# Optimization experiments

Hardware: AMD Instinct MI355X
Metric: run time of the kernel (lower is better)

## Reference

```python
import jax, jax.numpy as jnp
import numpy as np
from jax import lax

B, L, ENC_IN, MARK = 8, 512, 7, 4
D_MODEL, EXPAND, D_STATE, D_CONV = 512, 2, 16, 4
D_INNER = D_MODEL * EXPAND
DT_RANK = int(np.ceil(D_MODEL / 16))  # 32
PRED_LEN, C_OUT = 96, 7


def _positional_embedding(seq_len, d_model):
    pos = jnp.arange(seq_len, dtype=jnp.float32)[:, None]
    div = jnp.exp(jnp.arange(0, d_model, 2, dtype=jnp.float32) * (-np.log(10000.0) / d_model))
    pe = jnp.zeros((seq_len, d_model), dtype=jnp.float32)
    pe = pe.at[:, 0::2].set(jnp.sin(pos * div))
    pe = pe.at[:, 1::2].set(jnp.cos(pos * div))
    return pe  # [L, d_model]


def setup_inputs() -> dict:
    key = jax.random.key(0)
    ks = jax.random.split(key, 20)
    s = 0.02
    inp = {
        "x_enc": jax.random.normal(ks[0], (B, L, ENC_IN), jnp.float32),
        "x_mark_enc": jax.random.normal(ks[1], (B, L, MARK), jnp.float32),
        "x_dec": jax.random.normal(ks[2], (B, 144, ENC_IN), jnp.float32),
        "x_mark_dec": jax.random.normal(ks[3], (B, 144, MARK), jnp.float32),
        # DataEmbedding params
        "token_conv_w": jax.random.normal(ks[4], (D_MODEL, ENC_IN, 3), jnp.float32) * s,
        "temporal_w": jax.random.normal(ks[5], (D_MODEL, MARK), jnp.float32) * s,
        # Mamba params
        "in_proj_w": jax.random.normal(ks[6], (2 * D_INNER, D_MODEL), jnp.float32) * s,
        "conv1d_w": jax.random.normal(ks[7], (D_INNER, 1, D_CONV), jnp.float32) * s,
        "conv1d_b": jnp.zeros((D_INNER,), jnp.float32),
        "x_proj_w": jax.random.normal(ks[8], (DT_RANK + 2 * D_STATE, D_INNER), jnp.float32) * s,
        "dt_proj_w": jax.random.normal(ks[9], (D_INNER, DT_RANK), jnp.float32) * s,
        "dt_proj_b": jax.random.normal(ks[10], (D_INNER,), jnp.float32) * s,
        "A_log": jnp.log(jnp.broadcast_to(jnp.arange(1, D_STATE + 1, dtype=jnp.float32), (D_INNER, D_STATE))),
        "D_param": jnp.ones((D_INNER,), jnp.float32),
        "out_proj_w": jax.random.normal(ks[11], (D_MODEL, D_INNER), jnp.float32) * s,
        # prediction head
        "head_w": jax.random.normal(ks[12], (PRED_LEN * C_OUT, D_MODEL), jnp.float32) * s,
        "head_b": jnp.zeros((PRED_LEN * C_OUT,), jnp.float32),
    }
    return inp


def reference(x_enc, x_mark_enc, x_dec, x_mark_dec, token_conv_w, temporal_w,
              in_proj_w, conv1d_w, conv1d_b, x_proj_w, dt_proj_w, dt_proj_b,
              A_log, D_param, out_proj_w, head_w, head_b):
    # --- instance normalization (mean/std detached as in torch) ---
    mean_enc = lax.stop_gradient(jnp.mean(x_enc, axis=1, keepdims=True))       # [B,1,C]
    xc = x_enc - mean_enc
    std_enc = lax.stop_gradient(jnp.sqrt(jnp.var(xc, axis=1, keepdims=True) + 1e-5))
    xn = xc / std_enc                                                          # [B,L,C]

    # --- DataEmbedding: circular conv token emb + timeF linear + sinusoidal PE ---
    xp = jnp.pad(xn, ((0, 0), (1, 1), (0, 0)), mode="wrap")                    # circular pad on L
    val = lax.conv_general_dilated(xp.transpose(0, 2, 1), token_conv_w, (1,), "VALID")  # [B,D,L]
    val = val.transpose(0, 2, 1)                                               # [B,L,D]
    temp = x_mark_enc @ temporal_w.T                                           # [B,L,D]
    x = val + temp + _positional_embedding(L, D_MODEL)[None]                   # [B,L,D]

    # --- Mamba block ---
    xz = x @ in_proj_w.T                                                       # [B,L,2*Di]
    x_part, z = jnp.split(xz, 2, axis=-1)
    # causal depthwise conv over time
    xt = jnp.pad(x_part.transpose(0, 2, 1), ((0, 0), (0, 0), (D_CONV - 1, 0)))
    xconv = lax.conv_general_dilated(xt, conv1d_w, (1,), "VALID",
                                     feature_group_count=D_INNER) + conv1d_b[None, :, None]
    u = jax.nn.silu(xconv.transpose(0, 2, 1))                                  # [B,L,Di]

    dbl = u @ x_proj_w.T                                                       # [B,L,dt_rank+2n]
    dt_low = dbl[..., :DT_RANK]
    Bm = dbl[..., DT_RANK:DT_RANK + D_STATE]                                   # [B,L,n]
    Cm = dbl[..., DT_RANK + D_STATE:]                                          # [B,L,n]
    dt = jax.nn.softplus(dt_low @ dt_proj_w.T + dt_proj_b)                     # [B,L,Di]

    A = -jnp.exp(A_log)                                                        # [Di,n]
    deltaA = jnp.exp(dt[..., None] * A)                                        # [B,L,Di,n]
    deltaBu = dt[..., None] * Bm[:, :, None, :] * u[..., None]                 # [B,L,Di,n]

    def step(h, inputs):
        dA_t, dBu_t, c_t = inputs                                              # [B,Di,n],[B,Di,n],[B,n]
        h = dA_t * h + dBu_t
        y_t = jnp.einsum("bdn,bn->bd", h, c_t)
        return h, y_t

    h0 = jnp.zeros((B, D_INNER, D_STATE), dtype=x.dtype)
    _, ys = lax.scan(step, h0, (deltaA.transpose(1, 0, 2, 3),
                                deltaBu.transpose(1, 0, 2, 3),
                                Cm.transpose(1, 0, 2)))
    y = ys.transpose(1, 0, 2) + u * D_param                                    # [B,L,Di]
    y = y * jax.nn.silu(z)
    x_out = y @ out_proj_w.T                                                   # [B,L,D]

    # --- prediction head on last hidden state ---
    last = x_out[:, -1, :]                                                     # [B,D]
    pred = (last @ head_w.T + head_b).reshape(-1, PRED_LEN, C_OUT)
    return pred * std_enc + mean_enc
```

## Files before the change

kernel.cpp:

```cpp
#include <hip/hip_runtime.h>
#include <hip/hip_bf16.h>
#include <math.h>

#define BB 8
#define LL 512
#define CIN 7
#define MARKN 4
#define DM 512
#define DI 1024
#define DSN 16
#define NOUTC 672
#define NTC 8

typedef unsigned short ushortT;
typedef __attribute__((ext_vector_type(8))) short short8v;
typedef __attribute__((ext_vector_type(4))) float f32x4;

__device__ __forceinline__ float bf2f(ushortT u){ return __uint_as_float(((unsigned)u)<<16); }
__device__ __forceinline__ ushortT f2bf(float f){ __hip_bfloat16 h = __float2bfloat16(f); return *(ushortT*)&h; }

__global__ __launch_bounds__(256) void k_prep(const float* __restrict__ w_in,
    const float* __restrict__ xpw, const float* __restrict__ xe,
    ushortT* __restrict__ wbf, ushortT* __restrict__ xpwbf,
    float* __restrict__ mean, float* __restrict__ stdv, float* __restrict__ xn){
  int blk = blockIdx.x, tid = threadIdx.x;
  if(blk < 1024){
    int i = (blk*256 + tid)*4;
    float4 v = *(const float4*)(w_in + i);
    ushort4 pk; pk.x=f2bf(v.x); pk.y=f2bf(v.y); pk.z=f2bf(v.z); pk.w=f2bf(v.w);
    *(ushort4*)(wbf + i) = pk;
  } else if(blk < 1088){
    int i = ((blk-1024)*256 + tid)*4;
    float4 v = *(const float4*)(xpw + i);
    ushort4 pk; pk.x=f2bf(v.x); pk.y=f2bf(v.y); pk.z=f2bf(v.z); pk.w=f2bf(v.w);
    *(ushort4*)(xpwbf + i) = pk;
  } else if(tid < 64){
    int bc = blk - 1088;
    int b = bc / CIN, c = bc % CIN;
    int t = tid;
    const float* base = xe + (b*LL)*CIN + c;
    float v[8]; float s = 0.f;
    #pragma unroll
    for(int i=0;i<8;i++){ v[i] = base[(t + i*64)*CIN]; s += v[i]; }
    #pragma unroll
    for(int o=32;o>=1;o>>=1) s += __shfl_down(s, o);
    float m = __shfl(s, 0) * (1.0f/LL);
    float vs = 0.f;
    #pragma unroll
    for(int i=0;i<8;i++){ float dv = v[i]-m; vs += dv*dv; }
    #pragma unroll
    for(int o=32;o>=1;o>>=1) vs += __shfl_down(vs, o);
    float var = __shfl(vs, 0) * (1.0f/LL);
    float sd = sqrtf(var + 1e-5f);
    float inv = 1.0f / sd;
    if(t == 0){ mean[bc] = m; stdv[bc] = sd; }
    float* xnb = xn + (b*LL)*CIN + c;
    #pragma unroll
    for(int i=0;i<8;i++) xnb[(t + i*64)*CIN] = (v[i]-m)*inv;
  }
}

__global__ __launch_bounds__(512) void k_embed(const float* __restrict__ xn,
    const float* __restrict__ xmark, const float* __restrict__ tw,
    const float* __restrict__ tpw, __hip_bfloat16* __restrict__ xo){
  __shared__ float sw[DM*21];
  __shared__ float sxr[10][CIN];
  __shared__ float smr[8][MARKN];
  int blk = blockIdx.x;
  int b = blk >> 6;
  int l0 = (blk & 63) << 3;
  int tid = threadIdx.x;
  for(int i=tid; i<DM*21; i+=512) sw[i] = tw[i];
  if(tid < 70){
    int r = tid / CIN, c = tid % CIN;
    int ls = (l0 - 1 + r + LL) % LL;
    sxr[r][c] = xn[(b*LL + ls)*CIN + c];
  } else if(tid >= 128 && tid < 160){
    int i2 = tid - 128; int r = i2 >> 2, m = i2 & 3;
    smr[r][m] = xmark[(b*LL + l0 + r)*MARKN + m];
  }
  __syncthreads();
  int d = tid;
  float wv[21];
  #pragma unroll
  for(int i=0;i<21;i++) wv[i] = sw[d*21 + i];
  float tv[4];
  #pragma unroll
  for(int m=0;m<4;m++) tv[m] = tpw[d*MARKN + m];
  float divv = expf((float)(2*(d>>1)) * (-0.0179889460390159843f));
  bool isodd = (d & 1) != 0;
  #pragma unroll
  for(int ll=0; ll<8; ll++){
    float acc = 0.f;
    #pragma unroll
    for(int c=0;c<CIN;c++){
      #pragma unroll
      for(int k=0;k<3;k++) acc += sxr[ll+k][c] * wv[c*3+k];
    }
    #pragma unroll
    for(int m=0;m<4;m++) acc += smr[ll][m] * tv[m];
    float ang = (float)(l0+ll) * divv;
    acc += isodd ? cosf(ang) : sinf(ang);
    xo[(size_t)(b*LL + l0 + ll)*DM + d] = __float2bfloat16(acc);
  }
}

__global__ __launch_bounds__(256) void k_inproj_mfma(const ushortT* __restrict__ A,
    const ushortT* __restrict__ Bw, ushortT* __restrict__ C){
  __shared__ ushortT Asl[2][128*64];
  __shared__ ushortT Bsl[2][128*64];
  int tid = threadIdx.x;
  int w = tid >> 6, l = tid & 63;
  int m0 = blockIdx.y * 128, n0 = blockIdx.x * 128;
  int wr = w >> 1, wc = w & 1;
  f32x4 acc[4][4] = {};
  int srow = l >> 3;
  int scolswz = ((l & 7) * 16) ^ (srow << 4);

#define IP_STAGE(bufi, kt) do{ \
    _Pragma("unroll") \
    for(int i=0;i<4;i++){ \
      int r0 = w*32 + i*8; \
      int r = r0 + srow; \
      const ushortT* gA = A + (size_t)(m0 + r)*512 + (kt)*64 + (scolswz>>1); \
      const ushortT* gB = Bw + (size_t)(n0 + r)*512 + (kt)*64 + (scolswz>>1); \
      __builtin_amdgcn_global_load_lds( \
        (const __attribute__((address_space(1))) unsigned int*)(const void*)gA, \
        (__attribute__((address_space(3))) unsigned int*)(void*)(Asl[bufi] + r0*64), 16, 0, 0); \
      __builtin_amdgcn_global_load_lds( \
        (const __attribute__((address_space(1))) unsigned int*)(const void*)gB, \
        (__attribute__((address_space(3))) unsigned int*)(void*)(Bsl[bufi] + r0*64), 16, 0, 0); \
    } }while(0)

  IP_STAGE(0, 0);
  __syncthreads();
  int cur = 0;
  for(int kt = 0; kt < 8; ++kt){
    if(kt < 7) IP_STAGE(cur^1, kt+1);
    #pragma unroll
    for(int kk=0;kk<2;kk++){
      short8v af[4], bfr[4];
      int cb = kk*64 + (l>>4)*16;
      #pragma unroll
      for(int mf=0;mf<4;mf++){
        int ar = wr*64 + mf*16 + (l&15);
        af[mf] = *(const short8v*)(Asl[cur] + ar*64 + ((cb ^ ((ar&7)<<4))>>1));
      }
      #pragma unroll
      for(int nf=0;nf<4;nf++){
        int br = wc*64 + nf*16 + (l&15);
        bfr[nf] = *(const short8v*)(Bsl[cur] + br*64 + ((cb ^ ((br&7)<<4))>>1));
      }
      #pragma unroll
      for(int mf=0;mf<4;mf++)
        #pragma unroll
        for(int nf=0;nf<4;nf++)
          acc[mf][nf] = __builtin_amdgcn_mfma_f32_16x16x32_bf16(af[mf], bfr[nf], acc[mf][nf], 0, 0, 0);
    }
    __syncthreads();
    cur ^= 1;
  }
#undef IP_STAGE
  #pragma unroll
  for(int mf=0;mf<4;mf++){
    int rbase = m0 + wr*64 + mf*16 + (l>>4)*4;
    #pragma unroll
    for(int nf=0;nf<4;nf++){
      int col = n0 + wc*64 + nf*16 + (l&15);
      #pragma unroll
      for(int r=0;r<4;r++)
        C[(size_t)(rbase+r)*1024 + col] = f2bf(acc[mf][nf][r]);
    }
  }
}

__global__ __launch_bounds__(1024) void k_dwconv(const ushortT* __restrict__ xpbf,
    const float* __restrict__ cw, const float* __restrict__ cb,
    ushortT* __restrict__ ubf){
  int blk = blockIdx.x;
  int b = blk >> 5, l0 = (blk & 31) * 16;
  int d = threadIdx.x;
  const float4 w4 = *(const float4*)(cw + d*4);
  float bias = cb[d];
  const ushortT* base = xpbf + (size_t)(b*LL + l0)*1024 + d;
  float x0=0.f, x1=0.f, x2=0.f;
  if(l0 > 0){
    x0 = bf2f(base[-3*1024]); x1 = bf2f(base[-2*1024]); x2 = bf2f(base[-1*1024]);
  }
  #pragma unroll
  for(int ll=0; ll<16; ++ll){
    float x3 = bf2f(base[(size_t)ll*1024]);
    float acc = bias + x0*w4.x + x1*w4.y + x2*w4.z + x3*w4.w;
    float s = acc / (1.f + __expf(-acc));
    ubf[(size_t)(b*LL + l0 + ll)*1024 + d] = f2bf(s);
    x0 = x1; x1 = x2; x2 = x3;
  }
}

__global__ __launch_bounds__(256) void k_xproj_mfma(const ushortT* __restrict__ A,
    const ushortT* __restrict__ Bw, float* __restrict__ C){
  __shared__ ushortT Asl[2][64*64];
  __shared__ ushortT Bsl[2][64*64];
  int tid = threadIdx.x;
  int w = tid >> 6, l = tid & 63;
  int m0 = blockIdx.x * 64;
  f32x4 acc[4] = {};
  int srow = l >> 3;
  int scol = ((l & 7) * 16) ^ (srow << 4);

#define XP_STAGE(bufi, kt) do{ \
    _Pragma("unroll") \
    for(int i=0;i<2;i++){ \
      int r0 = w*16 + i*8; \
      int r = r0 + srow; \
      const ushortT* gA = A + (size_t)(m0 + r)*1024 + (kt)*64 + (scol>>1); \
      const ushortT* gB = Bw + (size_t)r*1024 + (kt)*64 + (scol>>1); \
      __builtin_amdgcn_global_load_lds( \
        (const __attribute__((address_space(1))) unsigned int*)(const void*)gA, \
        (__attribute__((address_space(3))) unsigned int*)(void*)(Asl[bufi] + r0*64), 16, 0, 0); \
      __builtin_amdgcn_global_load_lds( \
        (const __attribute__((address_space(1))) unsigned int*)(const void*)gB, \
        (__attribute__((address_space(3))) unsigned int*)(void*)(Bsl[bufi] + r0*64), 16, 0, 0); \
    } }while(0)

  XP_STAGE(0, 0);
  __syncthreads();
  int cur = 0;
  for(int kt = 0; kt < 16; ++kt){
    if(kt < 15) XP_STAGE(cur^1, kt+1);
    #pragma unroll
    for(int kk=0;kk<2;kk++){
      int cb = kk*64 + (l>>4)*16;
      int ar = w*16 + (l&15);
      short8v af = *(const short8v*)(Asl[cur] + ar*64 + ((cb ^ ((ar&7)<<4))>>1));
      #pragma unroll
      for(int nf=0;nf<4;nf++){
        int br = nf*16 + (l&15);
        short8v bfv = *(const short8v*)(Bsl[cur] + br*64 + ((cb ^ ((br&7)<<4))>>1));
        acc[nf] = __builtin_amdgcn_mfma_f32_16x16x32_bf16(af, bfv, acc[nf], 0, 0, 0);
      }
    }
    __syncthreads();
    cur ^= 1;
  }
#undef XP_STAGE
  int rbase = m0 + w*16 + (l>>4)*4;
  #pragma unroll
  for(int nf=0;nf<4;nf++){
    int col = nf*16 + (l&15);
    #pragma unroll
    for(int r=0;r<4;r++)
      C[(size_t)(rbase+r)*64 + col] = acc[nf][r];
  }
}

__global__ __launch_bounds__(256) void k_scan_chunk(const float* __restrict__ dbl,
    const ushortT* __restrict__ ubf, const float* __restrict__ dtw,
    const float* __restrict__ dtb, const float* __restrict__ alog,
    float4* __restrict__ P4, float4* __restrict__ Q4){
  int tc = blockIdx.x;
  int dgrp = blockIdx.y;
  int b = blockIdx.z;
  int tid = threadIdx.x;
  int d = dgrp*256 + tid;
  __shared__ float sD[64][68];
  #pragma unroll
  for(int j=0;j<4;j++){
    int idx = j*256 + tid;
    int row = idx >> 4, q = idx & 15;
    float4 v = *(const float4*)(dbl + (size_t)(b*LL + tc*64 + row)*64 + q*4);
    *(float4*)(&sD[row][q*4]) = v;
  }
  float wdt[32];
  #pragma unroll
  for(int r4=0;r4<8;r4++){
    float4 v = *(const float4*)(dtw + (size_t)d*32 + r4*4);
    wdt[r4*4]=v.x; wdt[r4*4+1]=v.y; wdt[r4*4+2]=v.z; wdt[r4*4+3]=v.w;
  }
  float bias = dtb[d];
  float Ad[16];
  {
    float4 a0 = *(const float4*)(alog + d*16);
    float4 a1 = *(const float4*)(alog + d*16 + 4);
    float4 a2 = *(const float4*)(alog + d*16 + 8);
    float4 a3 = *(const float4*)(alog + d*16 + 12);
    Ad[0]=-__expf(a0.x); Ad[1]=-__expf(a0.y); Ad[2]=-__expf(a0.z); Ad[3]=-__expf(a0.w);
    Ad[4]=-__expf(a1.x); Ad[5]=-__expf(a1.y); Ad[6]=-__expf(a1.z); Ad[7]=-__expf(a1.w);
    Ad[8]=-__expf(a2.x); Ad[9]=-__expf(a2.y); Ad[10]=-__expf(a2.z); Ad[11]=-__expf(a2.w);
    Ad[12]=-__expf(a3.x); Ad[13]=-__expf(a3.y); Ad[14]=-__expf(a3.z); Ad[15]=-__expf(a3.w);
  }
  __syncthreads();
  float h[16];
  #pragma unroll
  for(int n=0;n<16;n++) h[n] = 0.f;
  float Ss = 0.f;
  const ushortT* up = ubf + (size_t)(b*LL + tc*64)*1024 + d;
  #pragma unroll 2
  for(int t=0;t<64;t++){
    float acc = bias;
    #pragma unroll
    for(int r=0;r<32;r++) acc += sD[t][r]*wdt[r];
    float dtv = (acc > 20.f) ? acc : __logf(1.f + __expf(acc));
    float uv = bf2f(up[(size_t)t*1024]);
    float wt = dtv * uv;
    Ss += dtv;
    #pragma unroll
    for(int n=0;n<16;n++){
      float e = __expf(dtv * Ad[n]);
      h[n] = h[n]*e + wt*sD[t][32+n];
    }
  }
  size_t base4 = (size_t)(tc*8 + b)*4*1024 + d;
  #pragma unroll
  for(int n4=0;n4<4;n4++){
    Q4[base4 + n4*1024] = make_float4(h[n4*4], h[n4*4+1], h[n4*4+2], h[n4*4+3]);
    P4[base4 + n4*1024] = make_float4(__expf(Ss*Ad[n4*4]), __expf(Ss*Ad[n4*4+1]),
                                      __expf(Ss*Ad[n4*4+2]), __expf(Ss*Ad[n4*4+3]));
  }
}

__global__ __launch_bounds__(64) void k_scan_combine(const float4* __restrict__ P4,
    const float4* __restrict__ Q4, const float* __restrict__ dbl,
    const ushortT* __restrict__ ubf, const ushortT* __restrict__ xbf,
    const ushortT* __restrict__ wbf, const float* __restrict__ Dp,
    float* __restrict__ yv){
  int gid = blockIdx.x*64 + threadIdx.x;
  int b = gid >> 10, d = gid & 1023;
  const ushortT* xr = xbf + (size_t)(b*LL + LL-1)*512;
  const ushortT* wr = wbf + (size_t)(1024 + d)*512;
  float zl = 0.f;
  for(int k=0;k<512;k+=8){
    short8v xv = *(const short8v*)(xr + k);
    short8v wv = *(const short8v*)(wr + k);
    #pragma unroll
    for(int j=0;j<8;j++) zl += bf2f((ushortT)xv[j])*bf2f((ushortT)wv[j]);
  }
  float h[16];
  #pragma unroll
  for(int n=0;n<16;n++) h[n] = 0.f;
  #pragma unroll
  for(int c=0;c<NTC;c++){
    size_t base4 = (size_t)(c*8 + b)*4*1024 + d;
    #pragma unroll
    for(int n4=0;n4<4;n4++){
      float4 pv = P4[base4 + n4*1024];
      float4 qv = Q4[base4 + n4*1024];
      h[n4*4+0] = pv.x*h[n4*4+0] + qv.x;
      h[n4*4+1] = pv.y*h[n4*4+1] + qv.y;
      h[n4*4+2] = pv.z*h[n4*4+2] + qv.z;
      h[n4*4+3] = pv.w*h[n4*4+3] + qv.w;
    }
  }
  const float* Crow = dbl + (size_t)(b*LL + LL-1)*64 + 48;
  float y = 0.f;
  #pragma unroll
  for(int n=0;n<16;n++) y += Crow[n]*h[n];
  float ul = bf2f(ubf[(size_t)(b*LL + LL-1)*1024 + d]);
  float sz = zl / (1.f + __expf(-zl));
  yv[b*1024 + d] = (y + ul*Dp[d]) * sz;
}

__global__ __launch_bounds__(256) void k_outproj(const float* __restrict__ yv,
    const float* __restrict__ W, float* __restrict__ xout){
  int tid = threadIdx.x;
  int j = blockIdx.x*8 + (tid>>5);
  int ks = tid & 31;
  float a[8] = {};
  #pragma unroll
  for(int t=0;t<8;t++){
    int k = ks*4 + t*128;
    float4 wv = *(const float4*)(W + (size_t)j*1024 + k);
    #pragma unroll
    for(int b=0;b<8;b++){
      float4 xv = *(const float4*)(yv + b*1024 + k);
      a[b] += xv.x*wv.x + xv.y*wv.y + xv.z*wv.z + xv.w*wv.w;
    }
  }
  #pragma unroll
  for(int b=0;b<8;b++){
    #pragma unroll
    for(int o=16;o>=1;o>>=1) a[b] += __shfl_xor(a[b], o);
  }
  if(ks==0){
    #pragma unroll
    for(int b=0;b<8;b++) xout[b*512 + j] = a[b];
  }
}

__global__ __launch_bounds__(256) void k_head(const float* __restrict__ xout,
    const float* __restrict__ W, const float* __restrict__ hb,
    const float* __restrict__ mean, const float* __restrict__ stdv,
    float* __restrict__ out){
  int tid = threadIdx.x;
  int o = blockIdx.x*8 + (tid>>5);
  int ks = tid & 31;
  float a[8] = {};
  #pragma unroll
  for(int t=0;t<4;t++){
    int k = ks*4 + t*128;
    float4 wv = *(const float4*)(W + (size_t)o*512 + k);
    #pragma unroll
    for(int b=0;b<8;b++){
      float4 xv = *(const float4*)(xout + b*512 + k);
      a[b] += xv.x*wv.x + xv.y*wv.y + xv.z*wv.z + xv.w*wv.w;
    }
  }
  #pragma unroll
  for(int b=0;b<8;b++){
    #pragma unroll
    for(int oo=16;oo>=1;oo>>=1) a[b] += __shfl_xor(a[b], oo);
  }
  if(ks==0){
    int c = o % 7;
    #pragma unroll
    for(int b=0;b<8;b++){
      float v = a[b] + hb[o];
      out[b*NOUTC + o] = v * stdv[b*CIN + c] + mean[b*CIN + c];
    }
  }
}

extern "C" void kernel_launch(void* const* d_in, const int* in_sizes, int n_in,
                              void* d_out, int out_size, void* d_ws, size_t ws_size,
                              hipStream_t stream) {
  const float* x_enc   = (const float*)d_in[0];
  const float* x_mark  = (const float*)d_in[1];
  const float* tconvw  = (const float*)d_in[4];
  const float* tempw   = (const float*)d_in[5];
  const float* inprojw = (const float*)d_in[6];
  const float* convw   = (const float*)d_in[7];
  const float* convb   = (const float*)d_in[8];
  const float* xprojw  = (const float*)d_in[9];
  const float* dtw     = (const float*)d_in[10];
  const float* dtb     = (const float*)d_in[11];
  const float* alog    = (const float*)d_in[12];
  const float* dpar    = (const float*)d_in[13];
  const float* outw    = (const float*)d_in[14];
  const float* headw   = (const float*)d_in[15];
  const float* headb   = (const float*)d_in[16];

  float* ws    = (float*)d_ws;
  float* mean  = ws;
  float* stdv  = ws + 64;
  float* xn    = ws + 128;
  ushortT* xbf = (ushortT*)(ws + 28800);
  ushortT* wbf = (ushortT*)(ws + 1077376);
  ushortT* xpwbf=(ushortT*)(ws + 1601664);
  ushortT* xpbf= (ushortT*)(ws + 1634432);
  ushortT* ubf = (ushortT*)(ws + 3731584);
  float* dbl   = ws + 5828736;
  float4* P4   = (float4*)(ws + 6090880);
  float4* Q4   = (float4*)(ws + 7139456);
  float* yv    = ws + 8188032;
  float* xout  = ws + 8196224;
  float* out   = (float*)d_out;

  k_prep  <<<1144, 256, 0, stream>>>(inprojw, xprojw, x_enc, wbf, xpwbf, mean, stdv, xn);
  k_embed <<<512, 512, 0, stream>>>(xn, x_mark, tconvw, tempw, (__hip_bfloat16*)xbf);
  k_inproj_mfma<<<dim3(8, 32), 256, 0, stream>>>(xbf, wbf, xpbf);
  k_dwconv<<<256, 1024, 0, stream>>>(xpbf, convw, convb, ubf);
  k_xproj_mfma<<<64, 256, 0, stream>>>(ubf, xpwbf, dbl);
  k_scan_chunk<<<dim3(NTC, 4, 8), 256, 0, stream>>>(dbl, ubf, dtw, dtb, alog, P4, Q4);
  k_scan_combine<<<128, 64, 0, stream>>>(P4, Q4, dbl, ubf, xbf, wbf, dpar, yv);
  k_outproj<<<64, 256, 0, stream>>>(yv, outw, xout);
  k_head  <<<84, 256, 0, stream>>>(xout, headw, headb, mean, stdv, out);
}
```

Before: 102.5 us.

## Fuse pipeline into five kernels and fold out_proj into head weights

Collapses nine launches into five. Normalization and embedding move into one front kernel, which also casts the weights and precomputes Weff = head_w·out_proj_w. The depthwise conv+SiLU is fused into the in_proj GEMM epilogue using a 16-row halo recomputed per tile. The x_proj GEMM is fused into the chunk-scan kernel via LDS, and the final output uses a single GEMV with Weff. This removes intermediate global round-trips and launch overhead, at the cost of redundant halo MFMA work and Weff computation on every call.

```diff
diff --git a/kernel.cpp b/kernel.cpp
--- a/kernel.cpp
+++ b/kernel.cpp
@@ -8,7 +8,6 @@
 #define MARKN 4
 #define DM 512
 #define DI 1024
-#define DSN 16
 #define NOUTC 672
 #define NTC 8
 
@@ -19,111 +18,257 @@
 __device__ __forceinline__ float bf2f(ushortT u){ return __uint_as_float(((unsigned)u)<<16); }
 __device__ __forceinline__ ushortT f2bf(float f){ __hip_bfloat16 h = __float2bfloat16(f); return *(ushortT*)&h; }
 
-__global__ __launch_bounds__(256) void k_prep(const float* __restrict__ w_in,
-    const float* __restrict__ xpw, const float* __restrict__ xe,
-    ushortT* __restrict__ wbf, ushortT* __restrict__ xpwbf,
-    float* __restrict__ mean, float* __restrict__ stdv, float* __restrict__ xn){
+__global__ __launch_bounds__(512) void k_front(const float* __restrict__ xe,
+    const float* __restrict__ xmark, const float* __restrict__ tw,
+    const float* __restrict__ tpw, const float* __restrict__ inprojw,
+    const float* __restrict__ xpw, const float* __restrict__ headw,
+    const float* __restrict__ outw,
+    __hip_bfloat16* __restrict__ xo, ushortT* __restrict__ wbf,
+    ushortT* __restrict__ xpwbf, float* __restrict__ Weff,
+    float* __restrict__ mean, float* __restrict__ stdv){
+  __shared__ __align__(16) char LDSF[65536];
   int blk = blockIdx.x, tid = threadIdx.x;
-  if(blk < 1024){
-    int i = (blk*256 + tid)*4;
-    float4 v = *(const float4*)(w_in + i);
+  if(blk < 512){
+    float* sw = (float*)LDSF;
+    float* sxr = (float*)(LDSF + 43008);
+    float* smr = (float*)(LDSF + 43328);
+    float* sMean = (float*)(LDSF + 43520);
+    float* sInv  = (float*)(LDSF + 43584);
+    int b = blk >> 6;
+    int l0 = (blk & 63) << 3;
+    int wv = tid >> 6, t2 = tid & 63;
+    if(wv < 7){
+      int c = wv;
+      const float* base = xe + (b*LL)*CIN + c;
+      float v[8]; float s = 0.f;
+      #pragma unroll
+      for(int i=0;i<8;i++){ v[i] = base[(t2 + i*64)*CIN]; s += v[i]; }
+      #pragma unroll
+      for(int o=32;o>=1;o>>=1) s += __shfl_down(s, o);
+      float m = __shfl(s, 0) * (1.0f/LL);
+      float vs = 0.f;
+      #pragma unroll
+      for(int i=0;i<8;i++){ float dv = v[i]-m; vs += dv*dv; }
+      #pragma unroll
+      for(int o=32;o>=1;o>>=1) vs += __shfl_down(vs, o);
+      float var = __shfl(vs, 0) * (1.0f/LL);
+      float sd = sqrtf(var + 1e-5f);
+      if(t2 == 0){
+        sMean[c] = m; sInv[c] = 1.0f/sd;
+        if(l0 == 0){ mean[b*CIN+c] = m; stdv[b*CIN+c] = sd; }
+      }
+    }
+    __syncthreads();
+    for(int i=tid; i<DM*21; i+=512) sw[i] = tw[i];
+    if(tid < 70){
+      int r = tid / CIN, c = tid % CIN;
+      int ls = (l0 - 1 + r + LL) % LL;
+      sxr[r*CIN+c] = (xe[(b*LL + ls)*CIN + c] - sMean[c]) * sInv[c];
+    } else if(tid >= 128 && tid < 160){
+      int i2 = tid - 128; int r = i2 >> 2, m = i2 & 3;
+      smr[r*MARKN+m] = xmark[(b*LL + l0 + r)*MARKN + m];
+    }
+    __syncthreads();
+    int d = tid;
+    float wv2[21];
+    #pragma unroll
+    for(int i=0;i<21;i++) wv2[i] = sw[d*21 + i];
+    float tv[4];
+    #pragma unroll
+    for(int m=0;m<4;m++) tv[m] = tpw[d*MARKN + m];
+    float divv = expf((float)(2*(d>>1)) * (-0.0179889460390159843f));
+    bool isodd = (d & 1) != 0;
+    #pragma unroll
+    for(int ll=0; ll<8; ll++){
+      float acc = 0.f;
+      #pragma unroll
+      for(int c=0;c<CIN;c++){
+        #pragma unroll
+        for(int k=0;k<3;k++) acc += sxr[(ll+k)*CIN+c] * wv2[c*3+k];
+      }
+      #pragma unroll
+      for(int m=0;m<4;m++) acc += smr[ll*MARKN+m] * tv[m];
+      float ang = (float)(l0+ll) * divv;
+      acc += isodd ? cosf(ang) : sinf(ang);
+      xo[(size_t)(b*LL + l0 + ll)*DM + d] = __float2bfloat16(acc);
+    }
+  } else if(blk < 1024){
+    int i = ((blk-512)*512 + tid)*4;
+    float4 v = *(const float4*)(inprojw + i);
     ushort4 pk; pk.x=f2bf(v.x); pk.y=f2bf(v.y); pk.z=f2bf(v.z); pk.w=f2bf(v.w);
     *(ushort4*)(wbf + i) = pk;
-  } else if(blk < 1088){
-    int i = ((blk-1024)*256 + tid)*4;
+  } else if(blk < 1056){
+    int i = ((blk-1024)*512 + tid)*4;
     float4 v = *(const float4*)(xpw + i);
     ushort4 pk; pk.x=f2bf(v.x); pk.y=f2bf(v.y); pk.z=f2bf(v.z); pk.w=f2bf(v.w);
     *(ushort4*)(xpwbf + i) = pk;
-  } else if(tid < 64){
-    int bc = blk - 1088;
-    int b = bc / CIN, c = bc % CIN;
-    int t = tid;
-    const float* base = xe + (b*LL)*CIN + c;
-    float v[8]; float s = 0.f;
-    #pragma unroll
-    for(int i=0;i<8;i++){ v[i] = base[(t + i*64)*CIN]; s += v[i]; }
-    #pragma unroll
-    for(int o=32;o>=1;o>>=1) s += __shfl_down(s, o);
-    float m = __shfl(s, 0) * (1.0f/LL);
-    float vs = 0.f;
-    #pragma unroll
-    for(int i=0;i<8;i++){ float dv = v[i]-m; vs += dv*dv; }
-    #pragma unroll
-    for(int o=32;o>=1;o>>=1) vs += __shfl_down(vs, o);
-    float var = __shfl(vs, 0) * (1.0f/LL);
-    float sd = sqrtf(var + 1e-5f);
-    float inv = 1.0f / sd;
-    if(t == 0){ mean[bc] = m; stdv[bc] = sd; }
-    float* xnb = xn + (b*LL)*CIN + c;
-    #pragma unroll
-    for(int i=0;i<8;i++) xnb[(t + i*64)*CIN] = (v[i]-m)*inv;
-  }
-}
-
-__global__ __launch_bounds__(512) void k_embed(const float* __restrict__ xn,
-    const float* __restrict__ xmark, const float* __restrict__ tw,
-    const float* __restrict__ tpw, __hip_bfloat16* __restrict__ xo){
-  __shared__ float sw[DM*21];
-  __shared__ float sxr[10][CIN];
-  __shared__ float smr[8][MARKN];
-  int blk = blockIdx.x;
-  int b = blk >> 6;
-  int l0 = (blk & 63) << 3;
-  int tid = threadIdx.x;
-  for(int i=tid; i<DM*21; i+=512) sw[i] = tw[i];
-  if(tid < 70){
-    int r = tid / CIN, c = tid % CIN;
-    int ls = (l0 - 1 + r + LL) % LL;
-    sxr[r][c] = xn[(b*LL + ls)*CIN + c];
-  } else if(tid >= 128 && tid < 160){
-    int i2 = tid - 128; int r = i2 >> 2, m = i2 & 3;
-    smr[r][m] = xmark[(b*LL + l0 + r)*MARKN + m];
-  }
-  __syncthreads();
-  int d = tid;
-  float wv[21];
-  #pragma unroll
-  for(int i=0;i<21;i++) wv[i] = sw[d*21 + i];
-  float tv[4];
-  #pragma unroll
-  for(int m=0;m<4;m++) tv[m] = tpw[d*MARKN + m];
-  float divv = expf((float)(2*(d>>1)) * (-0.0179889460390159843f));
-  bool isodd = (d & 1) != 0;
-  #pragma unroll
-  for(int ll=0; ll<8; ll++){
-    float acc = 0.f;
-    #pragma unroll
-    for(int c=0;c<CIN;c++){
-      #pragma unroll
-      for(int k=0;k<3;k++) acc += sxr[ll+k][c] * wv[c*3+k];
-    }
-    #pragma unroll
-    for(int m=0;m<4;m++) acc += smr[ll][m] * tv[m];
-    float ang = (float)(l0+ll) * divv;
-    acc += isodd ? cosf(ang) : sinf(ang);
-    xo[(size_t)(b*LL + l0 + ll)*DM + d] = __float2bfloat16(acc);
-  }
-}
-
-__global__ __launch_bounds__(256) void k_inproj_mfma(const ushortT* __restrict__ A,
-    const ushortT* __restrict__ Bw, ushortT* __restrict__ C){
-  __shared__ ushortT Asl[2][128*64];
-  __shared__ ushortT Bsl[2][128*64];
+  } else {
+    float* sHW = (float*)LDSF;
+    float* sRed = (float*)(LDSF + 32768);
+    int wb = blk - 1056;
+    int o0 = (wb >> 4) * 16, j0 = (wb & 15) * 64;
+    for(int i=tid; i<16*512; i+=512) sHW[i] = headw[(size_t)(o0 + (i>>9))*512 + (i & 511)];
+    __syncthreads();
+    int lane = tid & 63, og = tid >> 6;
+    float acc[16];
+    #pragma unroll
+    for(int o=0;o<16;o++) acc[o] = 0.f;
+    for(int kk=0;kk<64;kk++){
+      int k = og*64 + kk;
+      float wv3 = outw[(size_t)k*1024 + j0 + lane];
+      #pragma unroll
+      for(int o=0;o<16;o++) acc[o] += sHW[o*512 + k] * wv3;
+    }
+    __syncthreads();
+    #pragma unroll
+    for(int o=0;o<16;o++) sRed[(og*16 + o)*64 + lane] = acc[o];
+    __syncthreads();
+    #pragma unroll
+    for(int e=0;e<2;e++){
+      int idx = tid + e*512;
+      int o = idx >> 6, j = idx & 63;
+      float s = 0.f;
+      #pragma unroll
+      for(int og2=0;og2<8;og2++) s += sRed[(og2*16 + o)*64 + j];
+      Weff[(size_t)(o0 + o)*1024 + j0 + j] = s;
+    }
+  }
+}
+
+__global__ __launch_bounds__(256) void k_inproj_dw(const ushortT* __restrict__ A,
+    const ushortT* __restrict__ Bw, const float* __restrict__ cw,
+    const float* __restrict__ cb, ushortT* __restrict__ ubf){
+  __shared__ __align__(16) ushortT LDSI[2*144*64 + 2*128*64];
+#define ASLB(bufi) (LDSI + (bufi)*144*64)
+#define BSLB(bufi) (LDSI + 2*144*64 + (bufi)*128*64)
   int tid = threadIdx.x;
   int w = tid >> 6, l = tid & 63;
   int m0 = blockIdx.y * 128, n0 = blockIdx.x * 128;
   int wr = w >> 1, wc = w & 1;
+  int hbase = (m0 == 0) ? 0 : m0 - 16;
   f32x4 acc[4][4] = {};
+  f32x4 hacc[4] = {};
   int srow = l >> 3;
   int scolswz = ((l & 7) * 16) ^ (srow << 4);
 
-#define IP_STAGE(bufi, kt) do{ \
+#define IPD_STAGE(bufi, kt) do{ \
     _Pragma("unroll") \
     for(int i=0;i<4;i++){ \
       int r0 = w*32 + i*8; \
-      int r = r0 + srow; \
-      const ushortT* gA = A + (size_t)(m0 + r)*512 + (kt)*64 + (scolswz>>1); \
-      const ushortT* gB = Bw + (size_t)(n0 + r)*512 + (kt)*64 + (scolswz>>1); \
+      const ushortT* gA = A + (size_t)(m0 + r0 + srow)*512 + (kt)*64 + (scolswz>>1); \
+      const ushortT* gB = Bw + (size_t)(n0 + r0 + srow)*512 + (kt)*64 + (scolswz>>1); \
+      __builtin_amdgcn_global_load_lds( \
+        (const __attribute__((address_space(1))) unsigned int*)(const void*)gA, \
+        (__attribute__((address_space(3))) unsigned int*)(void*)(ASLB(bufi) + (16 + r0)*64), 16, 0, 0); \
+      __builtin_amdgcn_global_load_lds( \
+        (const __attribute__((address_space(1))) unsigned int*)(const void*)gB, \
+        (__attribute__((address_space(3))) unsigned int*)(void*)(BSLB(bufi) + r0*64), 16, 0, 0); \
+    } \
+    if(w < 2){ \
+      int hr0 = w*8; \
+      const ushortT* gH = A + (size_t)(hbase + hr0 + srow)*512 + (kt)*64 + (scolswz>>1); \
+      __builtin_amdgcn_global_load_lds( \
+        (const __attribute__((address_space(1))) unsigned int*)(const void*)gH, \
+        (__attribute__((address_space(3))) unsigned int*)(void*)(ASLB(bufi) + hr0*64), 16, 0, 0); \
+    } }while(0)
+
+  IPD_STAGE(0, 0);
+  __syncthreads();
+  int cur = 0;
+  for(int kt = 0; kt < 8; ++kt){
+    if(kt < 7) IPD_STAGE(cur^1, kt+1);
+    #pragma unroll
+    for(int kk=0;kk<2;kk++){
+      short8v af[4], bfr[4];
+      int cb2 = kk*64 + (l>>4)*16;
+      #pragma unroll
+      for(int mf=0;mf<4;mf++){
+        int ar = 16 + wr*64 + mf*16 + (l&15);
+        af[mf] = *(const short8v*)(ASLB(cur) + ar*64 + ((cb2 ^ ((ar&7)<<4))>>1));
+      }
+      #pragma unroll
+      for(int nf=0;nf<4;nf++){
+        int br = wc*64 + nf*16 + (l&15);
+        bfr[nf] = *(const short8v*)(BSLB(cur) + br*64 + ((cb2 ^ ((br&7)<<4))>>1));
+      }
+      #pragma unroll
+      for(int mf=0;mf<4;mf++)
+        #pragma unroll
+        for(int nf=0;nf<4;nf++)
+          acc[mf][nf] = __builtin_amdgcn_mfma_f32_16x16x32_bf16(af[mf], bfr[nf], acc[mf][nf], 0, 0, 0);
+      if(w < 2){
+        int har = (l&15);
+        short8v haf = *(const short8v*)(ASLB(cur) + har*64 + ((cb2 ^ ((har&7)<<4))>>1));
+        #pragma unroll
+        for(int nf=0;nf<4;nf++)
+          hacc[nf] = __builtin_amdgcn_mfma_f32_16x16x32_bf16(haf, bfr[nf], hacc[nf], 0, 0, 0);
+      }
+    }
+    __syncthreads();
+    cur ^= 1;
+  }
+#undef IPD_STAGE
+  ushortT* sU = LDSI;
+  const int US = 136;
+  #pragma unroll
+  for(int mf=0;mf<4;mf++){
+    int rb = 16 + wr*64 + mf*16 + (l>>4)*4;
+    #pragma unroll
+    for(int nf=0;nf<4;nf++){
+      int col = wc*64 + nf*16 + (l&15);
+      #pragma unroll
+      for(int r=0;r<4;r++) sU[(rb+r)*US + col] = f2bf(acc[mf][nf][r]);
+    }
+  }
+  if(w < 2){
+    int rb = (l>>4)*4;
+    #pragma unroll
+    for(int nf=0;nf<4;nf++){
+      int col = wc*64 + nf*16 + (l&15);
+      #pragma unroll
+      for(int r=0;r<4;r++) sU[(rb+r)*US + col] = f2bf(hacc[nf][r]);
+    }
+  }
+  __syncthreads();
+  int col = tid & 127, rh = tid >> 7;
+  const float4 w4 = *(const float4*)(cw + (size_t)(n0+col)*4);
+  float bias = cb[n0+col];
+  int lbase = m0 & 511;
+  for(int R = rh*64; R < rh*64 + 64; ++R){
+    int lg = lbase + R;
+    float x3 = bf2f(sU[(16+R)*US + col]);
+    float x2 = (lg>=1) ? bf2f(sU[(15+R)*US + col]) : 0.f;
+    float x1 = (lg>=2) ? bf2f(sU[(14+R)*US + col]) : 0.f;
+    float x0 = (lg>=3) ? bf2f(sU[(13+R)*US + col]) : 0.f;
+    float a = bias + x0*w4.x + x1*w4.y + x2*w4.z + x3*w4.w;
+    float s = a / (1.f + __expf(-a));
+    ubf[(size_t)(m0+R)*1024 + n0 + col] = f2bf(s);
+  }
+#undef ASLB
+#undef BSLB
+}
+
+__global__ __launch_bounds__(256) void k_xscan(const ushortT* __restrict__ Aub,
+    const ushortT* __restrict__ Bw, const float* __restrict__ dtw,
+    const float* __restrict__ dtb, const float* __restrict__ alog,
+    float4* __restrict__ P4, float4* __restrict__ Q4, float* __restrict__ Crow){
+  int tc = blockIdx.x, dgrp = blockIdx.y, b = blockIdx.z;
+  int tid = threadIdx.x;
+  int w = tid >> 6, l = tid & 63;
+  __shared__ ushortT Asl[2][64*64];
+  __shared__ ushortT Bsl[2][64*64];
+  __shared__ float sD[64][68];
+  int m0 = b*LL + tc*64;
+  f32x4 acc[4] = {};
+  int srow = l >> 3;
+  int scol = ((l & 7) * 16) ^ (srow << 4);
+
+#define XS_STAGE(bufi, kt) do{ \
+    _Pragma("unroll") \
+    for(int i=0;i<2;i++){ \
+      int r0 = w*16 + i*8; \
+      const ushortT* gA = Aub + (size_t)(m0 + r0 + srow)*1024 + (kt)*64 + (scol>>1); \
+      const ushortT* gB = Bw + (size_t)(r0 + srow)*1024 + (kt)*64 + (scol>>1); \
       __builtin_amdgcn_global_load_lds( \
         (const __attribute__((address_space(1))) unsigned int*)(const void*)gA, \
         (__attribute__((address_space(3))) unsigned int*)(void*)(Asl[bufi] + r0*64), 16, 0, 0); \
@@ -132,145 +277,39 @@
         (__attribute__((address_space(3))) unsigned int*)(void*)(Bsl[bufi] + r0*64), 16, 0, 0); \
     } }while(0)
 
-  IP_STAGE(0, 0);
-  __syncthreads();
-  int cur = 0;
-  for(int kt = 0; kt < 8; ++kt){
-    if(kt < 7) IP_STAGE(cur^1, kt+1);
-    #pragma unroll
-    for(int kk=0;kk<2;kk++){
-      short8v af[4], bfr[4];
-      int cb = kk*64 + (l>>4)*16;
-      #pragma unroll
-      for(int mf=0;mf<4;mf++){
-        int ar = wr*64 + mf*16 + (l&15);
-        af[mf] = *(const short8v*)(Asl[cur] + ar*64 + ((cb ^ ((ar&7)<<4))>>1));
-      }
-      #pragma unroll
-      for(int nf=0;nf<4;nf++){
-        int br = wc*64 + nf*16 + (l&15);
-        bfr[nf] = *(const short8v*)(Bsl[cur] + br*64 + ((cb ^ ((br&7)<<4))>>1));
-      }
-      #pragma unroll
-      for(int mf=0;mf<4;mf++)
-        #pragma unroll
-        for(int nf=0;nf<4;nf++)
-          acc[mf][nf] = __builtin_amdgcn_mfma_f32_16x16x32_bf16(af[mf], bfr[nf], acc[mf][nf], 0, 0, 0);
-    }
-    __syncthreads();
-    cur ^= 1;
-  }
-#undef IP_STAGE
-  #pragma unroll
-  for(int mf=0;mf<4;mf++){
-    int rbase = m0 + wr*64 + mf*16 + (l>>4)*4;
-    #pragma unroll
-    for(int nf=0;nf<4;nf++){
-      int col = n0 + wc*64 + nf*16 + (l&15);
-      #pragma unroll
-      for(int r=0;r<4;r++)
-        C[(size_t)(rbase+r)*1024 + col] = f2bf(acc[mf][nf][r]);
-    }
-  }
-}
-
-__global__ __launch_bounds__(1024) void k_dwconv(const ushortT* __restrict__ xpbf,
-    const float* __restrict__ cw, const float* __restrict__ cb,
-    ushortT* __restrict__ ubf){
-  int blk = blockIdx.x;
-  int b = blk >> 5, l0 = (blk & 31) * 16;
-  int d = threadIdx.x;
-  const float4 w4 = *(const float4*)(cw + d*4);
-  float bias = cb[d];
-  const ushortT* base = xpbf + (size_t)(b*LL + l0)*1024 + d;
-  float x0=0.f, x1=0.f, x2=0.f;
-  if(l0 > 0){
-    x0 = bf2f(base[-3*1024]); x1 = bf2f(base[-2*1024]); x2 = bf2f(base[-1*1024]);
-  }
-  #pragma unroll
-  for(int ll=0; ll<16; ++ll){
-    float x3 = bf2f(base[(size_t)ll*1024]);
-    float acc = bias + x0*w4.x + x1*w4.y + x2*w4.z + x3*w4.w;
-    float s = acc / (1.f + __expf(-acc));
-    ubf[(size_t)(b*LL + l0 + ll)*1024 + d] = f2bf(s);
-    x0 = x1; x1 = x2; x2 = x3;
-  }
-}
-
-__global__ __launch_bounds__(256) void k_xproj_mfma(const ushortT* __restrict__ A,
-    const ushortT* __restrict__ Bw, float* __restrict__ C){
-  __shared__ ushortT Asl[2][64*64];
-  __shared__ ushortT Bsl[2][64*64];
-  int tid = threadIdx.x;
-  int w = tid >> 6, l = tid & 63;
-  int m0 = blockIdx.x * 64;
-  f32x4 acc[4] = {};
-  int srow = l >> 3;
-  int scol = ((l & 7) * 16) ^ (srow << 4);
-
-#define XP_STAGE(bufi, kt) do{ \
-    _Pragma("unroll") \
-    for(int i=0;i<2;i++){ \
-      int r0 = w*16 + i*8; \
-      int r = r0 + srow; \
-      const ushortT* gA = A + (size_t)(m0 + r)*1024 + (kt)*64 + (scol>>1); \
-      const ushortT* gB = Bw + (size_t)r*1024 + (kt)*64 + (scol>>1); \
-      __builtin_amdgcn_global_load_lds( \
-        (const __attribute__((address_space(1))) unsigned int*)(const void*)gA, \
-        (__attribute__((address_space(3))) unsigned int*)(void*)(Asl[bufi] + r0*64), 16, 0, 0); \
-      __builtin_amdgcn_global_load_lds( \
-        (const __attribute__((address_space(1))) unsigned int*)(const void*)gB, \
-        (__attribute__((address_space(3))) unsigned int*)(void*)(Bsl[bufi] + r0*64), 16, 0, 0); \
-    } }while(0)
-
-  XP_STAGE(0, 0);
+  XS_STAGE(0, 0);
   __syncthreads();
   int cur = 0;
   for(int kt = 0; kt < 16; ++kt){
-    if(kt < 15) XP_STAGE(cur^1, kt+1);
+    if(kt < 15) XS_STAGE(cur^1, kt+1);
     #pragma unroll
     for(int kk=0;kk<2;kk++){
-      int cb = kk*64 + (l>>4)*16;
+      int cb2 = kk*64 + (l>>4)*16;
       int ar = w*16 + (l&15);
-      short8v af = *(const short8v*)(Asl[cur] + ar*64 + ((cb ^ ((ar&7)<<4))>>1));
+      short8v af = *(const short8v*)(Asl[cur] + ar*64 + ((cb2 ^ ((ar&7)<<4))>>1));
       #pragma unroll
       for(int nf=0;nf<4;nf++){
         int br = nf*16 + (l&15);
-        short8v bfv = *(const short8v*)(Bsl[cur] + br*64 + ((cb ^ ((br&7)<<4))>>1));
+        short8v bfv = *(const short8v*)(Bsl[cur] + br*64 + ((cb2 ^ ((br&7)<<4))>>1));
         acc[nf] = __builtin_amdgcn_mfma_f32_16x16x32_bf16(af, bfv, acc[nf], 0, 0, 0);
       }
     }
     __syncthreads();
     cur ^= 1;
   }
-#undef XP_STAGE
-  int rbase = m0 + w*16 + (l>>4)*4;
-  #pragma unroll
-  for(int nf=0;nf<4;nf++){
-    int col = nf*16 + (l&15);
-    #pragma unroll
-    for(int r=0;r<4;r++)
-      C[(size_t)(rbase+r)*64 + col] = acc[nf][r];
-  }
-}
-
-__global__ __launch_bounds__(256) void k_scan_chunk(const float* __restrict__ dbl,
-    const ushortT* __restrict__ ubf, const float* __restrict__ dtw,
-    const float* __restrict__ dtb, const float* __restrict__ alog,
-    float4* __restrict__ P4, float4* __restrict__ Q4){
-  int tc = blockIdx.x;
-  int dgrp = blockIdx.y;
-  int b = blockIdx.z;
-  int tid = threadIdx.x;
+#undef XS_STAGE
+  {
+    int rb = w*16 + (l>>4)*4;
+    #pragma unroll
+    for(int nf=0;nf<4;nf++){
+      int colx = nf*16 + (l&15);
+      #pragma unroll
+      for(int r=0;r<4;r++) sD[rb+r][colx] = acc[nf][r];
+    }
+  }
+  __syncthreads();
+  if(tc == 7 && tid < 16) Crow[b*16 + tid] = sD[63][48 + tid];
   int d = dgrp*256 + tid;
-  __shared__ float sD[64][68];
-  #pragma unroll
-  for(int j=0;j<4;j++){
-    int idx = j*256 + tid;
-    int row = idx >> 4, q = idx & 15;
-    float4 v = *(const float4*)(dbl + (size_t)(b*LL + tc*64 + row)*64 + q*4);
-    *(float4*)(&sD[row][q*4]) = v;
-  }
   float wdt[32];
   #pragma unroll
   for(int r4=0;r4<8;r4++){
@@ -289,18 +328,17 @@
     Ad[8]=-__expf(a2.x); Ad[9]=-__expf(a2.y); Ad[10]=-__expf(a2.z); Ad[11]=-__expf(a2.w);
     Ad[12]=-__expf(a3.x); Ad[13]=-__expf(a3.y); Ad[14]=-__expf(a3.z); Ad[15]=-__expf(a3.w);
   }
-  __syncthreads();
   float h[16];
   #pragma unroll
   for(int n=0;n<16;n++) h[n] = 0.f;
   float Ss = 0.f;
-  const ushortT* up = ubf + (size_t)(b*LL + tc*64)*1024 + d;
+  const ushortT* up = Aub + (size_t)m0*1024 + d;
   #pragma unroll 2
   for(int t=0;t<64;t++){
-    float acc = bias;
-    #pragma unroll
-    for(int r=0;r<32;r++) acc += sD[t][r]*wdt[r];
-    float dtv = (acc > 20.f) ? acc : __logf(1.f + __expf(acc));
+    float a2 = bias;
+    #pragma unroll
+    for(int r=0;r<32;r++) a2 += sD[t][r]*wdt[r];
+    float dtv = (a2 > 20.f) ? a2 : __logf(1.f + __expf(a2));
     float uv = bf2f(up[(size_t)t*1024]);
     float wt = dtv * uv;
     Ss += dtv;
@@ -320,7 +358,7 @@
 }
 
 __global__ __launch_bounds__(64) void k_scan_combine(const float4* __restrict__ P4,
-    const float4* __restrict__ Q4, const float* __restrict__ dbl,
+    const float4* __restrict__ Q4, const float* __restrict__ Crow,
     const ushortT* __restrict__ ubf, const ushortT* __restrict__ xbf,
     const ushortT* __restrict__ wbf, const float* __restrict__ Dp,
     float* __restrict__ yv){
@@ -351,44 +389,16 @@
       h[n4*4+3] = pv.w*h[n4*4+3] + qv.w;
     }
   }
-  const float* Crow = dbl + (size_t)(b*LL + LL-1)*64 + 48;
   float y = 0.f;
   #pragma unroll
-  for(int n=0;n<16;n++) y += Crow[n]*h[n];
+  for(int n=0;n<16;n++) y += Crow[b*16+n]*h[n];
   float ul = bf2f(ubf[(size_t)(b*LL + LL-1)*1024 + d]);
   float sz = zl / (1.f + __expf(-zl));
   yv[b*1024 + d] = (y + ul*Dp[d]) * sz;
 }
 
-__global__ __launch_bounds__(256) void k_outproj(const float* __restrict__ yv,
-    const float* __restrict__ W, float* __restrict__ xout){
-  int tid = threadIdx.x;
-  int j = blockIdx.x*8 + (tid>>5);
-  int ks = tid & 31;
-  float a[8] = {};
-  #pragma unroll
-  for(int t=0;t<8;t++){
-    int k = ks*4 + t*128;
-    float4 wv = *(const float4*)(W + (size_t)j*1024 + k);
-    #pragma unroll
-    for(int b=0;b<8;b++){
-      float4 xv = *(const float4*)(yv + b*1024 + k);
-      a[b] += xv.x*wv.x + xv.y*wv.y + xv.z*wv.z + xv.w*wv.w;
-    }
-  }
-  #pragma unroll
-  for(int b=0;b<8;b++){
-    #pragma unroll
-    for(int o=16;o>=1;o>>=1) a[b] += __shfl_xor(a[b], o);
-  }
-  if(ks==0){
-    #pragma unroll
-    for(int b=0;b<8;b++) xout[b*512 + j] = a[b];
-  }
-}
-
-__global__ __launch_bounds__(256) void k_head(const float* __restrict__ xout,
-    const float* __restrict__ W, const float* __restrict__ hb,
+__global__ __launch_bounds__(256) void k_final(const float* __restrict__ yv,
+    const float* __restrict__ Weff, const float* __restrict__ hb,
     const float* __restrict__ mean, const float* __restrict__ stdv,
     float* __restrict__ out){
   int tid = threadIdx.x;
@@ -396,12 +406,12 @@
   int ks = tid & 31;
   float a[8] = {};
   #pragma unroll
-  for(int t=0;t<4;t++){
+  for(int t=0;t<8;t++){
     int k = ks*4 + t*128;
-    float4 wv = *(const float4*)(W + (size_t)o*512 + k);
+    float4 wv = *(const float4*)(Weff + (size_t)o*1024 + k);
     #pragma unroll
     for(int b=0;b<8;b++){
-      float4 xv = *(const float4*)(xout + b*512 + k);
+      float4 xv = *(const float4*)(yv + b*1024 + k);
       a[b] += xv.x*wv.x + xv.y*wv.y + xv.z*wv.z + xv.w*wv.w;
     }
   }
@@ -442,26 +452,22 @@
   float* ws    = (float*)d_ws;
   float* mean  = ws;
   float* stdv  = ws + 64;
-  float* xn    = ws + 128;
-  ushortT* xbf = (ushortT*)(ws + 28800);
-  ushortT* wbf = (ushortT*)(ws + 1077376);
-  ushortT* xpwbf=(ushortT*)(ws + 1601664);
-  ushortT* xpbf= (ushortT*)(ws + 1634432);
-  ushortT* ubf = (ushortT*)(ws + 3731584);
-  float* dbl   = ws + 5828736;
-  float4* P4   = (float4*)(ws + 6090880);
-  float4* Q4   = (float4*)(ws + 7139456);
-  float* yv    = ws + 8188032;
-  float* xout  = ws + 8196224;
+  ushortT* xbf = (ushortT*)(ws + 128);
+  ushortT* wbf = (ushortT*)(ws + 1048704);
+  ushortT* xpwbf=(ushortT*)(ws + 1572992);
+  float* Weff  = ws + 1605760;
+  ushortT* ubf = (ushortT*)(ws + 2293888);
+  float4* P4   = (float4*)(ws + 4391040);
+  float4* Q4   = (float4*)(ws + 5439616);
+  float* yv    = ws + 6488192;
+  float* Crow  = ws + 6496384;
   float* out   = (float*)d_out;
 
-  k_prep  <<<1144, 256, 0, stream>>>(inprojw, xprojw, x_enc, wbf, xpwbf, mean, stdv, xn);
-  k_embed <<<512, 512, 0, stream>>>(xn, x_mark, tconvw, tempw, (__hip_bfloat16*)xbf);
-  k_inproj_mfma<<<dim3(8, 32), 256, 0, stream>>>(xbf, wbf, xpbf);
-  k_dwconv<<<256, 1024, 0, stream>>>(xpbf, convw, convb, ubf);
-  k_xproj_mfma<<<64, 256, 0, stream>>>(ubf, xpwbf, dbl);
-  k_scan_chunk<<<dim3(NTC, 4, 8), 256, 0, stream>>>(dbl, ubf, dtw, dtb, alog, P4, Q4);
-  k_scan_combine<<<128, 64, 0, stream>>>(P4, Q4, dbl, ubf, xbf, wbf, dpar, yv);
-  k_outproj<<<64, 256, 0, stream>>>(yv, outw, xout);
-  k_head  <<<84, 256, 0, stream>>>(xout, headw, headb, mean, stdv, out);
-}
+  k_front<<<1728, 512, 0, stream>>>(x_enc, x_mark, tconvw, tempw, inprojw, xprojw,
+                                    headw, outw, (__hip_bfloat16*)xbf, wbf, xpwbf,
+                                    Weff, mean, stdv);
+  k_inproj_dw<<<dim3(8, 32), 256, 0, stream>>>(xbf, wbf, convw, convb, ubf);
+  k_xscan<<<dim3(NTC, 4, 8), 256, 0, stream>>>(ubf, xpwbf, dtw, dtb, alog, P4, Q4, Crow);
+  k_scan_combine<<<128, 64, 0, stream>>>(P4, Q4, Crow, ubf, xbf, wbf, dpar, yv);
+  k_final<<<84, 256, 0, stream>>>(yv, Weff, headb, mean, stdv, out);
+}
```

Result: slower. 121.0 us (+18.1%).
